# Kernel optimization log

Hardware: AMD Instinct MI355X
Metric: run time of the kernel (lower is better)

The kernel has to match this reference:

```python
import jax, jax.numpy as jnp
import numpy as np

N_NODES = 100000
N_EDGES = 1600000
IN_CH = 128
HID_CH = 128   # 2 * out_channels
OUT_CH = 64


def _gcn_conv(x, W, b, src, dst, dinv, n_nodes):
    """PyG GCNConv: x @ W, then sym-normalized scatter-add over edges (self-loops included in src/dst), plus bias."""
    h = x @ W                                   # [N, F_out]
    norm = dinv[src] * dinv[dst]                # [E+N]
    msg = h[src] * norm[:, None]                # [E+N, F_out] -- dominant HBM traffic
    out = jax.ops.segment_sum(msg, dst, num_segments=n_nodes)
    return out + b


def setup_inputs() -> dict:
    key = jax.random.key(0)
    k1, k2, k3, k4 = jax.random.split(key, 4)
    x = jax.random.normal(k1, (N_NODES, IN_CH), dtype=jnp.float32)
    edge_index = jax.random.randint(k2, (2, N_EDGES), 0, N_NODES, dtype=jnp.int64)
    # glorot-ish scaled weights
    W1 = jax.random.normal(k3, (IN_CH, HID_CH), dtype=jnp.float32) * (1.0 / np.sqrt(IN_CH))
    b1 = jnp.zeros((HID_CH,), dtype=jnp.float32)
    W2 = jax.random.normal(k4, (HID_CH, OUT_CH), dtype=jnp.float32) * (1.0 / np.sqrt(HID_CH))
    b2 = jnp.zeros((OUT_CH,), dtype=jnp.float32)
    return {"x": x, "edge_index": edge_index, "W1": W1, "b1": b1, "W2": W2, "b2": b2}


def reference(x, edge_index, W1, b1, W2, b2):
    n = x.shape[0]
    loop = jnp.arange(n, dtype=edge_index.dtype)
    src = jnp.concatenate([edge_index[0], loop])   # add self-loops (GCNConv default)
    dst = jnp.concatenate([edge_index[1], loop])
    # symmetric normalization: deg counted on destination nodes (edge weight = 1)
    deg = jax.ops.segment_sum(jnp.ones_like(dst, dtype=x.dtype), dst, num_segments=n)
    dinv = jnp.where(deg > 0, jax.lax.rsqrt(jnp.maximum(deg, 1.0)), 0.0)
    # conv1 -> ReLU (DFALayer is identity in forward)
    h = jax.nn.relu(_gcn_conv(x, W1, b1, src, dst, dinv, n))
    # conv2 (DFA wrapper is identity in forward)
    return _gcn_conv(h, W2, b2, src, dst, dinv, n)
```

## Files before the change

### kernel.cpp

```cpp
#include <hip/hip_runtime.h>
#include <hip/hip_bf16.h>
#include <cstdint>

typedef short bf16x8 __attribute__((ext_vector_type(8)));
typedef float f32x4 __attribute__((ext_vector_type(4)));


__device__ inline float blo(uint u) { return __uint_as_float(u << 16); }
__device__ inline float bhi(uint u) { return __uint_as_float(u & 0xffff0000u); }
__device__ inline ushort f2bu(float x) {
    __hip_bfloat16 h = __float2bfloat16(x);
    return *reinterpret_cast<ushort*>(&h);
}
__device__ inline uint fpack2(float x, float y) {
    return (uint)f2bu(x) | ((uint)f2bu(y) << 16);
}


__global__ __launch_bounds__(256) void hist_k(const int* __restrict__ ei,
                                              uint* __restrict__ hist, int E, int n) {
    __shared__ uint h[256];
    int t = threadIdx.x, blk = blockIdx.x;
    int nb = (n + 511) >> 9;
    h[t] = 0;
    __syncthreads();
    int chunk = (E + 255) / 256;
    int e0 = blk * chunk, e1 = min(E, e0 + chunk);
    for (int e = e0 + t; e < e1; e += 256)
        atomicAdd(&h[((uint)ei[(size_t)E + e]) >> 9], 1u);
    __syncthreads();
    if (t < nb) hist[(size_t)t * 256 + blk] = h[t];
}

__global__ __launch_bounds__(256) void scanA_k(const uint* __restrict__ hist,
                                               uint* __restrict__ histex,
                                               uint* __restrict__ btot) {
    __shared__ uint s[256];
    int t = threadIdx.x, b = blockIdx.x;
    uint v = hist[(size_t)b * 256 + t];
    s[t] = v;
    __syncthreads();
    for (int off = 1; off < 256; off <<= 1) {
        uint u = (t >= off) ? s[t - off] : 0;
        __syncthreads();
        s[t] += u;
        __syncthreads();
    }
    histex[(size_t)b * 256 + t] = s[t] - v;
    if (t == 255) btot[b] = s[255];
}

__global__ __launch_bounds__(256) void scanB_k(const uint* __restrict__ btot,
                                               uint* __restrict__ bbase,
                                               int* __restrict__ rp, int n, int E) {
    __shared__ uint s[256];
    int t = threadIdx.x;
    int nb = (n + 511) >> 9;
    uint v = (t < nb) ? btot[t] : 0;
    s[t] = v;
    __syncthreads();
    for (int off = 1; off < 256; off <<= 1) {
        uint u = (t >= off) ? s[t - off] : 0;
        __syncthreads();
        s[t] += u;
        __syncthreads();
    }
    if (t < nb) bbase[t] = s[t] - v;
    if (t == nb - 1) bbase[nb] = s[t];
    if (t == 0) rp[n] = E;
}

__global__ __launch_bounds__(256) void scat_k(const int* __restrict__ ei,
                                              const uint* __restrict__ bbase,
                                              const uint* __restrict__ histex,
                                              uint* __restrict__ pairs, int E, int n) {
    __shared__ uint cur[256];
    int t = threadIdx.x, blk = blockIdx.x;
    int nb = (n + 511) >> 9;
    if (t < nb) cur[t] = bbase[t] + histex[(size_t)t * 256 + blk];
    __syncthreads();
    int chunk = (E + 255) / 256;
    int e0 = blk * chunk, e1 = min(E, e0 + chunk);
    for (int e = e0 + t; e < e1; e += 256) {
        uint src = (uint)ei[e];
        uint dst = (uint)ei[(size_t)E + e];
        uint p = atomicAdd(&cur[dst >> 9], 1u);
        pairs[p] = (src << 9) | (dst & 511u);
    }
}

__global__ __launch_bounds__(256) void build_k(const uint* __restrict__ pairs,
                                               const uint* __restrict__ bbase,
                                               int* __restrict__ rp,
                                               float* __restrict__ dinv,
                                               int* __restrict__ eb, int n) {
    __shared__ uint lcnt[512];
    __shared__ uint lsc[256];
    int t = threadIdx.x, b = blockIdx.x;
    uint e0 = bbase[b], e1 = bbase[b + 1];
    lcnt[t] = 0;
    lcnt[t + 256] = 0;
    __syncthreads();
    for (uint e = e0 + t; e < e1; e += 256)
        atomicAdd(&lcnt[pairs[e] & 511u], 1u);
    __syncthreads();
    uint c0 = lcnt[2 * t], c1 = lcnt[2 * t + 1];
    uint sm = c0 + c1;
    lsc[t] = sm;
    __syncthreads();
    for (int off = 1; off < 256; off <<= 1) {
        uint u = (t >= off) ? lsc[t - off] : 0;
        __syncthreads();
        lsc[t] += u;
        __syncthreads();
    }
    uint ex = lsc[t] - sm;
    int node0 = (b << 9) + 2 * t;
    if (node0 < n) {
        rp[node0] = (int)(e0 + ex);
        dinv[node0] = rsqrtf((float)(c0 + 1));
    }
    if (node0 + 1 < n) {
        rp[node0 + 1] = (int)(e0 + ex + c0);
        dinv[node0 + 1] = rsqrtf((float)(c1 + 1));
    }
    lcnt[2 * t] = e0 + ex;
    lcnt[2 * t + 1] = e0 + ex + c0;
    __syncthreads();
    for (uint e = e0 + t; e < e1; e += 256) {
        uint p = pairs[e];
        uint pos = atomicAdd(&lcnt[p & 511u], 1u);
        eb[pos] = (int)(p >> 9);
    }
}


template <int OUTC, bool INB>
__global__ __launch_bounds__(256) void mgemm_k(const void* __restrict__ Xv,
                                               const float* __restrict__ W,
                                               const float* __restrict__ dinv,
                                               uint* __restrict__ outb, int n) {
    constexpr int WOFF = 32768;
    constexpr int C4 = OUTC / 4;
    constexpr int NC = OUTC / 16;
    constexpr int LDSB = (32768 + OUTC * 256) > (128 * OUTC * 4)
                             ? (32768 + OUTC * 256) : (128 * OUTC * 4);
    __shared__ uint4 ldsv[LDSB / 16];
    char* lds = (char*)ldsv;

    int t = threadIdx.x;
    int r0b = blockIdx.x * 128;

    for (int i = t; i < 128 * C4; i += 256) {
        int k = i / C4, c0 = (i % C4) * 4;
        float4 w = ((const float4*)W)[i];
        const float* wf = (const float*)&w;
#pragma unroll
        for (int j = 0; j < 4; ++j) {
            int c = c0 + j;
            *(ushort*)(lds + WOFF + c * 256 + ((k * 2) ^ ((c & 7) << 4))) = f2bu(wf[j]);
        }
    }
    if constexpr (!INB) {
        for (int i = t; i < 128 * 32; i += 256) {
            int r = i >> 5, kq = i & 31;
            uint2 p = make_uint2(0u, 0u);
            if (r0b + r < n) {
                float4 v = ((const float4*)Xv)[(size_t)(r0b + r) * 32 + kq];
                p = make_uint2(fpack2(v.x, v.y), fpack2(v.z, v.w));
            }
            *(uint2*)(lds + r * 256 + ((kq * 8) ^ ((r & 7) << 4))) = p;
        }
    } else {
        for (int i = t; i < 128 * 16; i += 256) {
            int r = i >> 4, kq = i & 15;
            uint4 p = make_uint4(0u, 0u, 0u, 0u);
            if (r0b + r < n) p = ((const uint4*)Xv)[(size_t)(r0b + r) * 16 + kq];
            *(uint4*)(lds + r * 256 + ((kq * 16) ^ ((r & 7) << 4))) = p;
        }
    }
    __syncthreads();

    int wv = t >> 6, lane = t & 63;
    int l15 = lane & 15, lg = lane >> 4;
    int wr0 = wv * 32;
    int swz = (l15 & 7) << 4;

    f32x4 acc[2][NC];
#pragma unroll
    for (int r = 0; r < 2; ++r)
#pragma unroll
        for (int cj = 0; cj < NC; ++cj) acc[r][cj] = (f32x4){0.f, 0.f, 0.f, 0.f};

#pragma unroll
    for (int kk = 0; kk < 4; ++kk) {
        int koff = kk * 64 + lg * 16;
        bf16x8 a0 = *(bf16x8*)(lds + (wr0 + l15) * 256 + (koff ^ swz));
        bf16x8 a1 = *(bf16x8*)(lds + (wr0 + 16 + l15) * 256 + (koff ^ swz));
#pragma unroll
        for (int cj = 0; cj < NC; ++cj) {
            int c = cj * 16 + l15;
            bf16x8 bv = *(bf16x8*)(lds + WOFF + c * 256 + (koff ^ swz));
            acc[0][cj] = __builtin_amdgcn_mfma_f32_16x16x32_bf16(a0, bv, acc[0][cj], 0, 0, 0);
            acc[1][cj] = __builtin_amdgcn_mfma_f32_16x16x32_bf16(a1, bv, acc[1][cj], 0, 0, 0);
        }
    }
    __syncthreads();

#pragma unroll
    for (int r = 0; r < 2; ++r)
#pragma unroll
        for (int cj = 0; cj < NC; ++cj) {
            int row = wr0 + r * 16 + lg * 4;
            int col = cj * 16 + l15;
#pragma unroll
            for (int j = 0; j < 4; ++j)
                *(float*)(lds + ((size_t)(row + j) * OUTC + col) * 4) = acc[r][cj][j];
        }
    __syncthreads();

    for (int i = t; i < 128 * C4; i += 256) {
        int r = i / C4, c4 = (i % C4) * 4;
        if (r0b + r < n) {
            float di = dinv[r0b + r];
            float4 d = *(float4*)(lds + (size_t)i * 16);
            uint2 p = make_uint2(fpack2(d.x * di, d.y * di), fpack2(d.z * di, d.w * di));
            *(uint2*)&outb[(size_t)(r0b + r) * (OUTC / 2) + (c4 >> 1)] = p;
        }
    }
}


__global__ __launch_bounds__(256) void agg128_k(const uint2* __restrict__ hs,
                                                const int* __restrict__ rp,
                                                const int* __restrict__ eb,
                                                const float* __restrict__ dinv,
                                                const float4* __restrict__ bias,
                                                uint2* __restrict__ outb, int n) {
    int wid = (blockIdx.x * 256 + threadIdx.x) >> 6;
    int lane = threadIdx.x & 63;
    if (wid >= n) return;
    int h = lane >> 5;
    int cq = lane & 31;
    int e0 = rp[wid], e1 = rp[wid + 1];
    const uint2* base = hs + cq;

    float a0 = 0.f, a1 = 0.f, a2 = 0.f, a3 = 0.f;
    if (h == 0) {
        uint2 s = base[(size_t)wid << 5];
        a0 = blo(s.x); a1 = bhi(s.x); a2 = blo(s.y); a3 = bhi(s.y);
    }

    int e = e0;
    for (; e + 16 <= e1; e += 16) {
        int s0 = eb[e + 0 + h], s1 = eb[e + 2 + h], s2 = eb[e + 4 + h], s3 = eb[e + 6 + h];
        int s4 = eb[e + 8 + h], s5 = eb[e + 10 + h], s6 = eb[e + 12 + h], s7 = eb[e + 14 + h];
        uint2 v0 = base[(size_t)s0 << 5];
        uint2 v1 = base[(size_t)s1 << 5];
        uint2 v2 = base[(size_t)s2 << 5];
        uint2 v3 = base[(size_t)s3 << 5];
        uint2 v4 = base[(size_t)s4 << 5];
        uint2 v5 = base[(size_t)s5 << 5];
        uint2 v6 = base[(size_t)s6 << 5];
        uint2 v7 = base[(size_t)s7 << 5];
        a0 += ((blo(v0.x) + blo(v1.x)) + (blo(v2.x) + blo(v3.x))) +
              ((blo(v4.x) + blo(v5.x)) + (blo(v6.x) + blo(v7.x)));
        a1 += ((bhi(v0.x) + bhi(v1.x)) + (bhi(v2.x) + bhi(v3.x))) +
              ((bhi(v4.x) + bhi(v5.x)) + (bhi(v6.x) + bhi(v7.x)));
        a2 += ((blo(v0.y) + blo(v1.y)) + (blo(v2.y) + blo(v3.y))) +
              ((blo(v4.y) + blo(v5.y)) + (blo(v6.y) + blo(v7.y)));
        a3 += ((bhi(v0.y) + bhi(v1.y)) + (bhi(v2.y) + bhi(v3.y))) +
              ((bhi(v4.y) + bhi(v5.y)) + (bhi(v6.y) + bhi(v7.y)));
    }
    for (; e + 2 <= e1; e += 2) {
        int s = eb[e + h];
        uint2 v = base[(size_t)s << 5];
        a0 += blo(v.x); a1 += bhi(v.x); a2 += blo(v.y); a3 += bhi(v.y);
    }
    if (e < e1 && h == 0) {
        uint2 v = base[(size_t)eb[e] << 5];
        a0 += blo(v.x); a1 += bhi(v.x); a2 += blo(v.y); a3 += bhi(v.y);
    }

    a0 += __shfl_xor(a0, 32, 64);
    a1 += __shfl_xor(a1, 32, 64);
    a2 += __shfl_xor(a2, 32, 64);
    a3 += __shfl_xor(a3, 32, 64);

    if (h == 0) {
        float di = dinv[wid];
        float4 b = bias[cq];
        uint2 p = make_uint2(fpack2(fmaxf(a0 * di + b.x, 0.f), fmaxf(a1 * di + b.y, 0.f)),
                             fpack2(fmaxf(a2 * di + b.z, 0.f), fmaxf(a3 * di + b.w, 0.f)));
        outb[((size_t)wid << 5) + cq] = p;
    }
}


__global__ __launch_bounds__(256) void agg64_k(const uint2* __restrict__ hs,
                                               const int* __restrict__ rp,
                                               const int* __restrict__ eb,
                                               const float* __restrict__ dinv,
                                               const float4* __restrict__ bias,
                                               float4* __restrict__ out, int n) {
    int wid = (blockIdx.x * 256 + threadIdx.x) >> 6;
    int lane = threadIdx.x & 63;
    if (wid >= n) return;
    int h = lane >> 4;
    int cq = lane & 15;
    int e0 = rp[wid], e1 = rp[wid + 1];
    const uint2* base = hs + cq;

    float a0 = 0.f, a1 = 0.f, a2 = 0.f, a3 = 0.f;
    if (h == 0) {
        uint2 s = base[(size_t)wid << 4];
        a0 = blo(s.x); a1 = bhi(s.x); a2 = blo(s.y); a3 = bhi(s.y);
    }

    int e = e0;
    for (; e + 16 <= e1; e += 16) {
        int s0 = eb[e + 0 + h], s1 = eb[e + 4 + h], s2 = eb[e + 8 + h], s3 = eb[e + 12 + h];
        uint2 v0 = base[(size_t)s0 << 4];
        uint2 v1 = base[(size_t)s1 << 4];
        uint2 v2 = base[(size_t)s2 << 4];
        uint2 v3 = base[(size_t)s3 << 4];
        a0 += (blo(v0.x) + blo(v1.x)) + (blo(v2.x) + blo(v3.x));
        a1 += (bhi(v0.x) + bhi(v1.x)) + (bhi(v2.x) + bhi(v3.x));
        a2 += (blo(v0.y) + blo(v1.y)) + (blo(v2.y) + blo(v3.y));
        a3 += (bhi(v0.y) + bhi(v1.y)) + (bhi(v2.y) + bhi(v3.y));
    }
    for (; e + 4 <= e1; e += 4) {
        int s = eb[e + h];
        uint2 v = base[(size_t)s << 4];
        a0 += blo(v.x); a1 += bhi(v.x); a2 += blo(v.y); a3 += bhi(v.y);
    }
    if (e + h < e1) {
        uint2 v = base[(size_t)eb[e + h] << 4];
        a0 += blo(v.x); a1 += bhi(v.x); a2 += blo(v.y); a3 += bhi(v.y);
    }

    a0 += __shfl_xor(a0, 16, 64);
    a1 += __shfl_xor(a1, 16, 64);
    a2 += __shfl_xor(a2, 16, 64);
    a3 += __shfl_xor(a3, 16, 64);
    a0 += __shfl_xor(a0, 32, 64);
    a1 += __shfl_xor(a1, 32, 64);
    a2 += __shfl_xor(a2, 32, 64);
    a3 += __shfl_xor(a3, 32, 64);

    if (h == 0) {
        float di = dinv[wid];
        float4 b = bias[cq];
        out[((size_t)wid << 4) + cq] =
            make_float4(a0 * di + b.x, a1 * di + b.y, a2 * di + b.z, a3 * di + b.w);
    }
}


extern "C" void kernel_launch(void* const* d_in, const int* in_sizes, int n_in,
                              void* d_out, int out_size, void* d_ws, size_t ws_size,
                              hipStream_t stream) {
    const float* x  = (const float*)d_in[0];
    const int*   ei = (const int*)d_in[1];
    const float* W1 = (const float*)d_in[2];
    const float* b1 = (const float*)d_in[3];
    const float* W2 = (const float*)d_in[4];
    const float* b2 = (const float*)d_in[5];
    float* out = (float*)d_out;

    int n = in_sizes[0] / 128;
    int E = in_sizes[1] / 2;
    int nb = (n + 511) >> 9;

    char* ws = (char*)d_ws;
    size_t o = 0;
    auto alloc = [&](size_t bytes) {
        size_t r = o;
        o = (o + bytes + 255) & ~(size_t)255;
        return r;
    };
    uint*  hist   = (uint*)(ws + alloc((size_t)256 * 256 * 4));
    uint*  histex = (uint*)(ws + alloc((size_t)256 * 256 * 4));
    uint*  btot   = (uint*)(ws + alloc(256 * 4));
    uint*  bbase  = (uint*)(ws + alloc(257 * 4));
    int*   rp     = (int*)(ws + alloc((size_t)(n + 1) * 4));
    float* dinv   = (float*)(ws + alloc((size_t)n * 4));
    uint*  pairs  = (uint*)(ws + alloc((size_t)E * 4));
    int*   eb     = (int*)(ws + alloc((size_t)E * 4));
    uint*  h1s    = (uint*)(ws + alloc((size_t)n * 64 * 4));
    uint*  a1     = (uint*)(ws + alloc((size_t)n * 64 * 4));
    uint*  h2s    = (uint*)(ws + alloc((size_t)n * 32 * 4));

    int gB = (n + 127) / 128;
    int gW = (int)(((size_t)n * 64 + 255) / 256);

    hist_k<<<256, 256, 0, stream>>>(ei, hist, E, n);
    scanA_k<<<nb, 256, 0, stream>>>(hist, histex, btot);
    scanB_k<<<1, 256, 0, stream>>>(btot, bbase, rp, n, E);
    scat_k<<<256, 256, 0, stream>>>(ei, bbase, histex, pairs, E, n);
    build_k<<<nb, 256, 0, stream>>>(pairs, bbase, rp, dinv, eb, n);

    mgemm_k<128, false><<<gB, 256, 0, stream>>>(x, W1, dinv, h1s, n);
    agg128_k<<<gW, 256, 0, stream>>>((const uint2*)h1s, rp, eb, dinv,
                                     (const float4*)b1, (uint2*)a1, n);
    mgemm_k<64, true><<<gB, 256, 0, stream>>>(a1, W2, dinv, h2s, n);
    agg64_k<<<gW, 256, 0, stream>>>((const uint2*)h2s, rp, eb, dinv,
                                    (const float4*)b2, (float4*)out, n);
}
```

Before: 233.2 us.

## Split GCN aggregation by feature-column groups with edge-parallel lanes

Rewrites both aggregation kernels so each block handles one of eight feature-column slices for a chunk of 64 destination nodes. Within a wave, lanes are spread across edges (16 or 32 at a time) instead of across features, and the partial sums are reduced with cross-lane xor shuffles. The aim is to narrow each block's gather footprint for better cache reuse and more memory parallelism per wave. In exchange, each gathered row is fetched in narrower pieces by multiple blocks, the edge-index list is read eight times, and the shuffle reduction is longer.

```diff
diff --git a/kernel.cpp b/kernel.cpp
--- a/kernel.cpp
+++ b/kernel.cpp
@@ -231,128 +231,92 @@
 }
 
 
-__global__ __launch_bounds__(256) void agg128_k(const uint2* __restrict__ hs,
+template <int DPB>
+__global__ __launch_bounds__(256) void agg128g_k(const uint2* __restrict__ hs,
+                                                 const int* __restrict__ rp,
+                                                 const int* __restrict__ eb,
+                                                 const float* __restrict__ dinv,
+                                                 const float4* __restrict__ bias,
+                                                 uint2* __restrict__ outb, int n) {
+    int g = blockIdx.x & 7;
+    int chunk = blockIdx.x >> 3;
+    int wave = threadIdx.x >> 6, lane = threadIdx.x & 63;
+    int cq = lane & 3;
+    int slot = lane >> 2;
+    const uint2* base = hs + g * 4 + cq;
+    float4 b = bias[g * 4 + cq];
+
+    int d0 = chunk * DPB;
+    int dend = min(n, d0 + DPB);
+    for (int d = d0 + wave; d < dend; d += 4) {
+        int e0 = rp[d], e1 = rp[d + 1];
+        float a0 = 0.f, a1 = 0.f, a2 = 0.f, a3 = 0.f;
+        for (int e = e0; e < e1; e += 16) {
+            int idx = e + slot;
+            uint2 v = make_uint2(0u, 0u);
+            if (idx < e1) v = base[(size_t)eb[idx] << 5];
+            a0 += blo(v.x); a1 += bhi(v.x); a2 += blo(v.y); a3 += bhi(v.y);
+        }
+#pragma unroll
+        for (int m = 4; m < 64; m <<= 1) {
+            a0 += __shfl_xor(a0, m, 64);
+            a1 += __shfl_xor(a1, m, 64);
+            a2 += __shfl_xor(a2, m, 64);
+            a3 += __shfl_xor(a3, m, 64);
+        }
+        if (slot == 0) {
+            uint2 s = base[(size_t)d << 5];
+            a0 += blo(s.x); a1 += bhi(s.x); a2 += blo(s.y); a3 += bhi(s.y);
+            float di = dinv[d];
+            uint2 p = make_uint2(
+                fpack2(fmaxf(a0 * di + b.x, 0.f), fmaxf(a1 * di + b.y, 0.f)),
+                fpack2(fmaxf(a2 * di + b.z, 0.f), fmaxf(a3 * di + b.w, 0.f)));
+            outb[((size_t)d << 5) + g * 4 + cq] = p;
+        }
+    }
+}
+
+
+template <int DPB>
+__global__ __launch_bounds__(256) void agg64g_k(const uint2* __restrict__ hs,
                                                 const int* __restrict__ rp,
                                                 const int* __restrict__ eb,
                                                 const float* __restrict__ dinv,
                                                 const float4* __restrict__ bias,
-                                                uint2* __restrict__ outb, int n) {
-    int wid = (blockIdx.x * 256 + threadIdx.x) >> 6;
-    int lane = threadIdx.x & 63;
-    if (wid >= n) return;
-    int h = lane >> 5;
-    int cq = lane & 31;
-    int e0 = rp[wid], e1 = rp[wid + 1];
-    const uint2* base = hs + cq;
-
-    float a0 = 0.f, a1 = 0.f, a2 = 0.f, a3 = 0.f;
-    if (h == 0) {
-        uint2 s = base[(size_t)wid << 5];
-        a0 = blo(s.x); a1 = bhi(s.x); a2 = blo(s.y); a3 = bhi(s.y);
-    }
-
-    int e = e0;
-    for (; e + 16 <= e1; e += 16) {
-        int s0 = eb[e + 0 + h], s1 = eb[e + 2 + h], s2 = eb[e + 4 + h], s3 = eb[e + 6 + h];
-        int s4 = eb[e + 8 + h], s5 = eb[e + 10 + h], s6 = eb[e + 12 + h], s7 = eb[e + 14 + h];
-        uint2 v0 = base[(size_t)s0 << 5];
-        uint2 v1 = base[(size_t)s1 << 5];
-        uint2 v2 = base[(size_t)s2 << 5];
-        uint2 v3 = base[(size_t)s3 << 5];
-        uint2 v4 = base[(size_t)s4 << 5];
-        uint2 v5 = base[(size_t)s5 << 5];
-        uint2 v6 = base[(size_t)s6 << 5];
-        uint2 v7 = base[(size_t)s7 << 5];
-        a0 += ((blo(v0.x) + blo(v1.x)) + (blo(v2.x) + blo(v3.x))) +
-              ((blo(v4.x) + blo(v5.x)) + (blo(v6.x) + blo(v7.x)));
-        a1 += ((bhi(v0.x) + bhi(v1.x)) + (bhi(v2.x) + bhi(v3.x))) +
-              ((bhi(v4.x) + bhi(v5.x)) + (bhi(v6.x) + bhi(v7.x)));
-        a2 += ((blo(v0.y) + blo(v1.y)) + (blo(v2.y) + blo(v3.y))) +
-              ((blo(v4.y) + blo(v5.y)) + (blo(v6.y) + blo(v7.y)));
-        a3 += ((bhi(v0.y) + bhi(v1.y)) + (bhi(v2.y) + bhi(v3.y))) +
-              ((bhi(v4.y) + bhi(v5.y)) + (bhi(v6.y) + bhi(v7.y)));
-    }
-    for (; e + 2 <= e1; e += 2) {
-        int s = eb[e + h];
-        uint2 v = base[(size_t)s << 5];
-        a0 += blo(v.x); a1 += bhi(v.x); a2 += blo(v.y); a3 += bhi(v.y);
-    }
-    if (e < e1 && h == 0) {
-        uint2 v = base[(size_t)eb[e] << 5];
-        a0 += blo(v.x); a1 += bhi(v.x); a2 += blo(v.y); a3 += bhi(v.y);
-    }
-
-    a0 += __shfl_xor(a0, 32, 64);
-    a1 += __shfl_xor(a1, 32, 64);
-    a2 += __shfl_xor(a2, 32, 64);
-    a3 += __shfl_xor(a3, 32, 64);
-
-    if (h == 0) {
-        float di = dinv[wid];
-        float4 b = bias[cq];
-        uint2 p = make_uint2(fpack2(fmaxf(a0 * di + b.x, 0.f), fmaxf(a1 * di + b.y, 0.f)),
-                             fpack2(fmaxf(a2 * di + b.z, 0.f), fmaxf(a3 * di + b.w, 0.f)));
-        outb[((size_t)wid << 5) + cq] = p;
-    }
-}
-
-
-__global__ __launch_bounds__(256) void agg64_k(const uint2* __restrict__ hs,
-                                               const int* __restrict__ rp,
-                                               const int* __restrict__ eb,
-                                               const float* __restrict__ dinv,
-                                               const float4* __restrict__ bias,
-                                               float4* __restrict__ out, int n) {
-    int wid = (blockIdx.x * 256 + threadIdx.x) >> 6;
-    int lane = threadIdx.x & 63;
-    if (wid >= n) return;
-    int h = lane >> 4;
-    int cq = lane & 15;
-    int e0 = rp[wid], e1 = rp[wid + 1];
-    const uint2* base = hs + cq;
-
-    float a0 = 0.f, a1 = 0.f, a2 = 0.f, a3 = 0.f;
-    if (h == 0) {
-        uint2 s = base[(size_t)wid << 4];
-        a0 = blo(s.x); a1 = bhi(s.x); a2 = blo(s.y); a3 = bhi(s.y);
-    }
-
-    int e = e0;
-    for (; e + 16 <= e1; e += 16) {
-        int s0 = eb[e + 0 + h], s1 = eb[e + 4 + h], s2 = eb[e + 8 + h], s3 = eb[e + 12 + h];
-        uint2 v0 = base[(size_t)s0 << 4];
-        uint2 v1 = base[(size_t)s1 << 4];
-        uint2 v2 = base[(size_t)s2 << 4];
-        uint2 v3 = base[(size_t)s3 << 4];
-        a0 += (blo(v0.x) + blo(v1.x)) + (blo(v2.x) + blo(v3.x));
-        a1 += (bhi(v0.x) + bhi(v1.x)) + (bhi(v2.x) + bhi(v3.x));
-        a2 += (blo(v0.y) + blo(v1.y)) + (blo(v2.y) + blo(v3.y));
-        a3 += (bhi(v0.y) + bhi(v1.y)) + (bhi(v2.y) + bhi(v3.y));
-    }
-    for (; e + 4 <= e1; e += 4) {
-        int s = eb[e + h];
-        uint2 v = base[(size_t)s << 4];
-        a0 += blo(v.x); a1 += bhi(v.x); a2 += blo(v.y); a3 += bhi(v.y);
-    }
-    if (e + h < e1) {
-        uint2 v = base[(size_t)eb[e + h] << 4];
-        a0 += blo(v.x); a1 += bhi(v.x); a2 += blo(v.y); a3 += bhi(v.y);
-    }
-
-    a0 += __shfl_xor(a0, 16, 64);
-    a1 += __shfl_xor(a1, 16, 64);
-    a2 += __shfl_xor(a2, 16, 64);
-    a3 += __shfl_xor(a3, 16, 64);
-    a0 += __shfl_xor(a0, 32, 64);
-    a1 += __shfl_xor(a1, 32, 64);
-    a2 += __shfl_xor(a2, 32, 64);
-    a3 += __shfl_xor(a3, 32, 64);
-
-    if (h == 0) {
-        float di = dinv[wid];
-        float4 b = bias[cq];
-        out[((size_t)wid << 4) + cq] =
-            make_float4(a0 * di + b.x, a1 * di + b.y, a2 * di + b.z, a3 * di + b.w);
+                                                float4* __restrict__ out, int n) {
+    int g = blockIdx.x & 7;
+    int chunk = blockIdx.x >> 3;
+    int wave = threadIdx.x >> 6, lane = threadIdx.x & 63;
+    int cq = lane & 1;
+    int slot = lane >> 1;
+    const uint2* base = hs + g * 2 + cq;
+    float4 b = bias[g * 2 + cq];
+
+    int d0 = chunk * DPB;
+    int dend = min(n, d0 + DPB);
+    for (int d = d0 + wave; d < dend; d += 4) {
+        int e0 = rp[d], e1 = rp[d + 1];
+        float a0 = 0.f, a1 = 0.f, a2 = 0.f, a3 = 0.f;
+        for (int e = e0; e < e1; e += 32) {
+            int idx = e + slot;
+            uint2 v = make_uint2(0u, 0u);
+            if (idx < e1) v = base[(size_t)eb[idx] << 4];
+            a0 += blo(v.x); a1 += bhi(v.x); a2 += blo(v.y); a3 += bhi(v.y);
+        }
+#pragma unroll
+        for (int m = 2; m < 64; m <<= 1) {
+            a0 += __shfl_xor(a0, m, 64);
+            a1 += __shfl_xor(a1, m, 64);
+            a2 += __shfl_xor(a2, m, 64);
+            a3 += __shfl_xor(a3, m, 64);
+        }
+        if (slot == 0) {
+            uint2 s = base[(size_t)d << 4];
+            a0 += blo(s.x); a1 += bhi(s.x); a2 += blo(s.y); a3 += bhi(s.y);
+            float di = dinv[d];
+            out[((size_t)d << 4) + g * 2 + cq] =
+                make_float4(a0 * di + b.x, a1 * di + b.y, a2 * di + b.z, a3 * di + b.w);
+        }
     }
 }
 
@@ -392,7 +356,8 @@
     uint*  h2s    = (uint*)(ws + alloc((size_t)n * 32 * 4));
 
     int gB = (n + 127) / 128;
-    int gW = (int)(((size_t)n * 64 + 255) / 256);
+    constexpr int DPB = 64;
+    int gG = 8 * ((n + DPB - 1) / DPB);
 
     hist_k<<<256, 256, 0, stream>>>(ei, hist, E, n);
     scanA_k<<<nb, 256, 0, stream>>>(hist, histex, btot);
@@ -401,9 +366,9 @@
     build_k<<<nb, 256, 0, stream>>>(pairs, bbase, rp, dinv, eb, n);
 
     mgemm_k<128, false><<<gB, 256, 0, stream>>>(x, W1, dinv, h1s, n);
-    agg128_k<<<gW, 256, 0, stream>>>((const uint2*)h1s, rp, eb, dinv,
-                                     (const float4*)b1, (uint2*)a1, n);
+    agg128g_k<DPB><<<gG, 256, 0, stream>>>((const uint2*)h1s, rp, eb, dinv,
+                                           (const float4*)b1, (uint2*)a1, n);
     mgemm_k<64, true><<<gB, 256, 0, stream>>>(a1, W2, dinv, h2s, n);
-    agg64_k<<<gW, 256, 0, stream>>>((const uint2*)h2s, rp, eb, dinv,
-                                    (const float4*)b2, (float4*)out, n);
-}
+    agg64g_k<DPB><<<gG, 256, 0, stream>>>((const uint2*)h2s, rp, eb, dinv,
+                                          (const float4*)b2, (float4*)out, n);
+}
```

Result: slower. 558.2 us (+139.3%).
